# Performance work log

Measured on AMD Instinct MI355X. Metric: run time of the kernel, lower is better.

The kernel has to match this reference:

```python
import jax, jax.numpy as jnp
import numpy as np

B, L, D, H, HD = 2, 8192, 1024, 16, 64
MINI = 64
NC = L // MINI
TTT_BASE_LR = 1.0
NUM_CHUNKS = 4
TEXT_LEN = 64
INIT_OFFSET = 2048


def setup_inputs() -> dict:
    key = jax.random.key(0)
    ks = jax.random.split(key, 16)
    hidden_states = jax.random.normal(ks[0], (B, L, D), dtype=jnp.float32)
    # llama-style rope table as (cos, sin) pairs: [L, HD//2, 2]
    inv_freq = 1.0 / (10000.0 ** (np.arange(0, HD, 2, dtype=np.float32) / HD))
    t = np.arange(L, dtype=np.float32)
    ang = np.outer(t, inv_freq)  # [L, HD//2]
    freqs_cis = jnp.asarray(np.stack([np.cos(ang), np.sin(ang)], axis=-1))
    std = 0.02
    inp = {"hidden_states": hidden_states, "freqs_cis": freqs_cis}
    names = ["wq", "wk", "wv", "wu"]
    for i, n in enumerate(names):
        inp[n + "_w"] = jax.random.normal(ks[1 + i], (D, D), dtype=jnp.float32) * std  # [in, out]
        inp[n + "_b"] = jnp.zeros((D,), dtype=jnp.float32)
    inp["ttt_norm_weight"] = jnp.ones((H, HD), dtype=jnp.float32)
    inp["ttt_norm_bias"] = jnp.zeros((H, HD), dtype=jnp.float32)
    inp["lr_weight"] = jax.random.normal(ks[6], (H, 1, D), dtype=jnp.float32) * std
    inp["lr_bias"] = jnp.zeros((H, 1), dtype=jnp.float32)
    return inp


def _l2norm(x):
    return x / jnp.maximum(jnp.linalg.norm(x, axis=-1, keepdims=True), 1e-12)


def _rope(x, cos, sin):
    # x: [B, L, H, HD]; cos/sin: [L, HD//2] -> broadcast [1, L, 1, HD//2]
    c = cos[None, :, None, :]
    s = sin[None, :, None, :]
    xr, xi = x[..., 0::2], x[..., 1::2]
    out_r = xr * c - xi * s
    out_i = xr * s + xi * c
    return jnp.stack([out_r, out_i], axis=-1).reshape(x.shape)


def _interleave(x):
    # x: [B, H, NC, C, F]; splice text chunks into video scenes (static offsets)
    b, h, nc, c, f = x.shape
    xf = x.reshape(b, h, nc * c, f)
    stl = TEXT_LEN * NUM_CHUNKS
    x_text = xf[:, :, :stl]
    x_video = xf[:, :, stl:]
    texts = jnp.split(x_text, NUM_CHUNKS, axis=2)
    vio = INIT_OFFSET - TEXT_LEN
    vids = [x_video[:, :, :vio]] + list(jnp.split(x_video[:, :, vio:], NUM_CHUNKS - 1, axis=2))
    pieces = [jnp.concatenate([texts[i], vids[i]], axis=2) for i in range(NUM_CHUNKS)]
    return jnp.concatenate(pieces, axis=2).reshape(b, h, nc, c, f)


def reference(hidden_states, freqs_cis, wq_w, wq_b, wk_w, wk_b, wv_w, wv_b,
              wu_w, wu_b, ttt_norm_weight, ttt_norm_bias, lr_weight, lr_bias):
    X = hidden_states  # [B, L, D]
    XQ = (X @ wq_w + wq_b).reshape(B, L, H, HD)
    XK = (X @ wk_w + wk_b).reshape(B, L, H, HD)
    XV = (X @ wv_w + wv_b).reshape(B, L, H, HD)
    XU = (X @ wu_w + wu_b).reshape(B, L, H, HD)

    XQ, XK, XU = _l2norm(XQ), _l2norm(XK), _l2norm(XU)

    # seq_text_length = 0 in process_input -> rope over the whole sequence
    cos, sin = freqs_cis[..., 0], freqs_cis[..., 1]
    XQ = _rope(XQ, cos, sin)
    XK = _rope(XK, cos, sin)
    XU = _rope(XU, cos, sin)

    # ln reconstruction target (std uses Bessel correction like torch.std)
    diff = XV - XK
    mean = diff.mean(axis=-1, keepdims=True)
    std = jnp.std(diff, axis=-1, keepdims=True, ddof=1)
    norm = (diff - mean) / (std + 1e-8)
    XV = ttt_norm_weight[None, None] * norm + ttt_norm_bias[None, None] + XK

    # reshape to mini-batches: [B, H, NC, C, HD]
    def to_mb(t):
        return t.transpose(0, 2, 1, 3).reshape(B, H, NC, MINI, HD)
    XQ, XK, XV, XU = to_mb(XQ), to_mb(XK), to_mb(XV), to_mb(XU)
    Xmb = X.reshape(B, NC, MINI, D)

    # per-head LR gating
    ttt_lr = jnp.einsum('bnkc,hdc->bhnkd', Xmb, lr_weight) + lr_bias.reshape(1, -1, 1, 1, 1)
    ttt_lr = jax.nn.sigmoid(ttt_lr).transpose(0, 1, 2, 4, 3)  # [B, H, NC, 1, C]
    ttt_lr = TTT_BASE_LR * ttt_lr / HD
    eta = (1.0 / MINI) * jnp.tile(ttt_lr, (1, 1, 1, MINI, 1))  # [B, H, NC, C, C]

    XQ, XK, XV, XU = _interleave(XQ), _interleave(XK), _interleave(XV), _interleave(XU)
    eta = _interleave(eta)

    # HD == MINI == 64 so all five stack cleanly
    return jnp.stack([XQ, XK, XV, XU, eta], axis=0)
```

## Files before the change

### kernel.cpp

```cpp
#include <hip/hip_runtime.h>

typedef unsigned int u32;
typedef unsigned short u16;
typedef short short8v __attribute__((ext_vector_type(8)));
typedef float f32x4 __attribute__((ext_vector_type(4)));

#define ND 1024
#define NH 16
#define OUT_T ((size_t)16777216)

__device__ __forceinline__ u16 f2bf(float f) {
  u32 u = __float_as_uint(f);
  u32 r = u + 0x7fffu + ((u >> 16) & 1u);
  return (u16)(r >> 16);
}

__device__ __forceinline__ short8v pack8(float4 a, float4 b) {
  short8v v;
  v[0] = (short)f2bf(a.x); v[1] = (short)f2bf(a.y);
  v[2] = (short)f2bf(a.z); v[3] = (short)f2bf(a.w);
  v[4] = (short)f2bf(b.x); v[5] = (short)f2bf(b.y);
  v[6] = (short)f2bf(b.z); v[7] = (short)f2bf(b.w);
  return v;
}

__device__ __forceinline__ void st8(float* p, const float* v) {
  for (int i = 0; i < 2; ++i) {
    f32x4 t; t[0] = v[4*i]; t[1] = v[4*i+1]; t[2] = v[4*i+2]; t[3] = v[4*i+3];
    *(f32x4*)(p + 4*i) = t;
  }
}

__device__ __forceinline__ void gload16(const void* g, void* l) {
  __builtin_amdgcn_global_load_lds((const __attribute__((address_space(1))) void*)g,
                                   (__attribute__((address_space(3))) void*)l, 16, 0, 0);
}

__global__ void k_wt(const float* __restrict__ w0, const float* __restrict__ w1,
                     const float* __restrict__ w2, const float* __restrict__ w3,
                     u16* __restrict__ WT) {
  __shared__ float T[64][65];
  int bid = blockIdx.x;
  int w = bid >> 8;
  int tk = (bid >> 4) & 15, tc = bid & 15;
  const float* W = w == 0 ? w0 : w == 1 ? w1 : w == 2 ? w2 : w3;
  int k0 = tk << 6, c0 = tc << 6;
  int tid = threadIdx.x;
  for (int it = 0; it < 16; ++it) {
    int idx = it * 256 + tid;
    int kk = idx >> 6, cc = idx & 63;
    T[kk][cc] = W[(size_t)(k0 + kk) * ND + c0 + cc];
  }
  __syncthreads();
  for (int it = 0; it < 2; ++it) {
    int ci = it * 256 + tid;
    int cc = ci >> 3, k8 = ci & 7;
    int c = c0 + cc;
    short8v v;
    for (int j = 0; j < 8; ++j) v[j] = (short)f2bf(T[k8 * 8 + j][cc]);
    size_t off = ((size_t)(w * ND + c) << 10) + k0 + (((k8 ^ c) & 7) << 3);
    *(short8v*)(WT + off) = v;
  }
}

__global__ void k_xbf(const float* __restrict__ X, u16* __restrict__ Xb) {
  size_t i = ((size_t)blockIdx.x * 256 + threadIdx.x) * 8;
  float4 a = *(const float4*)(X + i), b = *(const float4*)(X + i + 4);
  *(short8v*)(Xb + i) = pack8(a, b);
}

__global__ __launch_bounds__(256) void k_lr2(const u16* __restrict__ Xb,
                                             const float* __restrict__ LW,
                                             const float* __restrict__ LB,
                                             float* __restrict__ out) {
  __shared__ __align__(16) char smem[46080];
  u16* LWs = (u16*)smem;
  u16* As = (u16*)(smem + 32768);
  float* El = (float*)(smem + 40960);
  const int tid = threadIdx.x, lane = tid & 63, wid = tid >> 6;
  const int l15 = lane & 15, lg = lane >> 4;
  const int n = blockIdx.x;
  const int tok0 = n << 6;

  {
    int row = tid >> 4;
    int cbase = (tid & 15) << 3;
    const float* src = LW + row * ND + (cbase << 3);
    for (int i = 0; i < 8; ++i) {
      float4 a = *(const float4*)(src + i * 8);
      float4 b = *(const float4*)(src + i * 8 + 4);
      int sc = (cbase + i) ^ (row & 7);
      *(short8v*)(LWs + row * 1024 + (sc << 3)) = pack8(a, b);
    }
  }

  const int arow0 = (wid << 4) + (lane >> 3);
  const u16* asrc = Xb + (size_t)(tok0 + arow0) * ND + ((((lane & 7) ^ arow0) & 7) << 3);
  const u32 aldo = wid << 10;
  const int aoff = ((wid << 4) + l15) << 6;
  const int key = l15 & 7;

  f32x4 acc;
  for (int r = 0; r < 4; ++r) acc[r] = 0.f;
  __syncthreads();

  for (int kt = 0; kt < 16; ++kt) {
    gload16(asrc + (kt << 6), As + aldo);
    gload16(asrc + (kt << 6) + 8 * ND, As + aldo + 512);
    __syncthreads();
    for (int ks = 0; ks < 2; ++ks) {
      int kcl = (ks << 2) + lg;
      int kcg = (kt << 3) + kcl;
      short8v af = *(const short8v*)(As + aoff + ((kcl ^ key) << 3));
      short8v bf = *(const short8v*)(LWs + (l15 << 10) + ((kcg ^ key) << 3));
      acc = __builtin_amdgcn_mfma_f32_16x16x32_bf16(af, bf, acc, 0, 0, 0);
    }
    __syncthreads();
  }

  for (int rr = 0; rr < 4; ++rr) {
    float v = acc[rr] + LB[l15];
    float e = (1.f / (1.f + expf(-v))) * (1.f / 4096.f);
    El[l15 * 72 + (wid << 4) + (lg << 2) + rr] = e;
  }
  __syncthreads();

  const int b = n >> 7, nl = n & 127;
  int q, rc;
  if (nl < 4) { q = nl; rc = 0; }
  else { q = (nl - 4) / 31; rc = nl - 3 - 31 * q; }
  const int pc = q * 32 + rc;
  const int j = tid >> 2, kq = tid & 3;
  size_t base = 4 * OUT_T + (((size_t)(b * NH) << 13) + (pc << 6)) * 64 + (size_t)j * 64;
  for (int h = 0; h < 16; ++h) {
    float* po = out + base + ((size_t)h << 19);
    for (int qq = 0; qq < 4; ++qq) {
      int k0 = (kq + (qq << 2)) << 2;
      const float* ep = El + h * 72 + k0;
      f32x4 t; t[0] = ep[0]; t[1] = ep[1]; t[2] = ep[2]; t[3] = ep[3];
      *(f32x4*)(po + k0) = t;
    }
  }
}

__global__ __launch_bounds__(512, 2) void k_main(
    const u16* __restrict__ Xb, const float* __restrict__ FC,
    const u16* __restrict__ WT,
    const float* __restrict__ qb, const float* __restrict__ kb,
    const float* __restrict__ vb, const float* __restrict__ ub,
    const float* __restrict__ tw, const float* __restrict__ tb,
    float* __restrict__ out) {
  __shared__ __align__(16) char smem[131072];
  float* Cs = (float*)smem;

  const int tid = threadIdx.x;
  const int lane = tid & 63;
  const int wid = tid >> 6;
  const int wm = wid >> 2, wn = wid & 3;
  const int l15 = lane & 15, lg = lane >> 4;
  const int xcd = blockIdx.x & 7;
  const int local = blockIdx.x >> 3;
  const int h = (xcd << 1) | (local >> 6);
  const int s0 = (local & 63) << 8;

  f32x4 acc[8][4];
  for (int i = 0; i < 8; ++i)
    for (int j = 0; j < 4; ++j)
      for (int r = 0; r < 4; ++r) acc[i][j][r] = 0.f;

  const float* bp = (wn == 0) ? qb : (wn == 1) ? kb : (wn == 2) ? vb : ub;
  float biasv[4];
  for (int fn = 0; fn < 4; ++fn) biasv[fn] = bp[h * 64 + fn * 16 + l15];

  const int arow0 = (wid << 5) + (lane >> 3);
  const u16* asrc = Xb + (size_t)(s0 + arow0) * ND + ((((lane & 7) ^ arow0) & 7) << 3);
  const u32 aldo = wid << 11;
  const int brow_d = ((wid & 1) << 5) + (lane >> 3);
  const u16* bsrc = WT + (((size_t)((wid >> 1) * ND + h * 64 + brow_d)) << 10) + ((lane & 7) << 3);
  const u32 bldo = wid << 11;

  int aoff[8], akey[8], boff[4], bkey[4];
  for (int f = 0; f < 8; ++f) {
    int ra = (wm << 7) + (f << 4) + l15;
    aoff[f] = ra << 6; akey[f] = ra & 7;
  }
  for (int f = 0; f < 4; ++f) {
    int rb = (wn << 6) + (f << 4) + l15;
    boff[f] = rb << 6; bkey[f] = rb & 7;
  }

  for (int j = 0; j < 4; ++j) {
    gload16(asrc + j * (8 * ND), (u16*)smem + aldo + (j << 9));
    gload16(bsrc + j * 8192, (u16*)(smem + 32768) + bldo + (j << 9));
  }
  __syncthreads();

  for (int kt = 0; kt < 16; ++kt) {
    const int cur = kt & 1;
    if (kt < 15) {
      const int k0 = (kt + 1) << 6;
      u16* ad = (u16*)(smem + ((cur ^ 1) << 16));
      u16* bd = (u16*)(smem + 32768 + ((cur ^ 1) << 16));
      for (int j = 0; j < 4; ++j) {
        gload16(asrc + k0 + j * (8 * ND), ad + aldo + (j << 9));
        gload16(bsrc + k0 + j * 8192, bd + bldo + (j << 9));
      }
    }
    const u16* As = (const u16*)(smem + (cur << 16));
    const u16* Bs = (const u16*)(smem + 32768 + (cur << 16));
    for (int ks = 0; ks < 2; ++ks) {
      const int kc = (ks << 2) + lg;
      short8v af[8], bf[4];
      for (int f = 0; f < 8; ++f)
        af[f] = *(const short8v*)(As + aoff[f] + ((kc ^ akey[f]) << 3));
      for (int f = 0; f < 4; ++f)
        bf[f] = *(const short8v*)(Bs + boff[f] + ((kc ^ bkey[f]) << 3));
      for (int fm = 0; fm < 8; ++fm)
        for (int fn = 0; fn < 4; ++fn)
          acc[fm][fn] = __builtin_amdgcn_mfma_f32_16x16x32_bf16(
              af[fm], bf[fn], acc[fm][fn], 0, 0, 0);
    }
    __syncthreads();
  }

  for (int ph = 0; ph < 4; ++ph) {
    if (wm == (ph >> 1)) {
      for (int f2 = 0; f2 < 4; ++f2) {
        int fm = ((ph & 1) << 2) + f2;
        for (int fn = 0; fn < 4; ++fn)
          for (int rr = 0; rr < 4; ++rr) {
            int rl = (f2 << 4) + (lg << 2) + rr;
            int col = (wn << 6) + (fn << 4) + l15;
            Cs[rl * 261 + col] = acc[fm][fn][rr] + biasv[fn];
          }
      }
    }
    __syncthreads();
    {
      int tloc = tid >> 3, o = tid & 7;
      int dbase = o << 3;
      int stok = s0 + (ph << 6) + tloc;
      int b = stok >> 13, seq = stok & 8191;
      const float* crow = Cs + tloc * 261;
      float fc[8];
      {
        const f32x4* fp = (const f32x4*)(FC + ((size_t)seq << 6) + dbase);
        f32x4 t0 = fp[0], t1 = fp[1];
        fc[0] = t0[0]; fc[1] = t0[1]; fc[2] = t0[2]; fc[3] = t0[3];
        fc[4] = t1[0]; fc[5] = t1[1]; fc[6] = t1[2]; fc[7] = t1[3];
      }
      float sq = 0.f, sk = 0.f, su = 0.f;
      for (int j = 0; j < 8; ++j) {
        float a = crow[dbase + j], b2 = crow[64 + dbase + j], c = crow[192 + dbase + j];
        sq += a * a; sk += b2 * b2; su += c * c;
      }
      sq += __shfl_xor(sq, 1); sq += __shfl_xor(sq, 2); sq += __shfl_xor(sq, 4);
      sk += __shfl_xor(sk, 1); sk += __shfl_xor(sk, 2); sk += __shfl_xor(sk, 4);
      su += __shfl_xor(su, 1); su += __shfl_xor(su, 2); su += __shfl_xor(su, 4);
      float qi = 1.f / fmaxf(sqrtf(sq), 1e-12f);
      float ki = 1.f / fmaxf(sqrtf(sk), 1e-12f);
      float ui = 1.f / fmaxf(sqrtf(su), 1e-12f);
      int p;
      if (seq < 256) p = ((seq >> 6) << 11) + (seq & 63);
      else { int v = seq - 256; int qc = v / 1984; p = (qc << 11) + 64 + (v - qc * 1984); }
      float* po = out + ((((size_t)(b * NH + h) << 13) + p) << 6) + dbase;
      float kr[8];
      for (int jj = 0; jj < 4; ++jj) {
        float xa = crow[64 + dbase + 2*jj] * ki, xb = crow[64 + dbase + 2*jj + 1] * ki;
        float c = fc[2*jj], s = fc[2*jj+1];
        kr[2*jj]     = xa * c - xb * s;
        kr[2*jj + 1] = xa * s + xb * c;
      }
      st8(po + OUT_T, kr);
      float sd = 0.f, sdd = 0.f, df[8];
      for (int j = 0; j < 8; ++j) {
        df[j] = crow[128 + dbase + j] - kr[j];
        sd += df[j]; sdd += df[j] * df[j];
      }
      sd += __shfl_xor(sd, 1); sd += __shfl_xor(sd, 2); sd += __shfl_xor(sd, 4);
      sdd += __shfl_xor(sdd, 1); sdd += __shfl_xor(sdd, 2); sdd += __shfl_xor(sdd, 4);
      float mean = sd * (1.f / 64.f);
      float var = (sdd - sd * sd * (1.f / 64.f)) * (1.f / 63.f);
      float istd = 1.f / (sqrtf(fmaxf(var, 0.f)) + 1e-8f);
      for (int j = 0; j < 8; ++j) {
        int d = dbase + j;
        df[j] = tw[h * 64 + d] * ((df[j] - mean) * istd) + tb[h * 64 + d] + kr[j];
      }
      st8(po + 2 * OUT_T, df);
      float qr[8];
      for (int jj = 0; jj < 4; ++jj) {
        float xa = crow[dbase + 2*jj] * qi, xb = crow[dbase + 2*jj + 1] * qi;
        float c = fc[2*jj], s = fc[2*jj+1];
        qr[2*jj]     = xa * c - xb * s;
        qr[2*jj + 1] = xa * s + xb * c;
      }
      st8(po, qr);
      for (int jj = 0; jj < 4; ++jj) {
        float xa = crow[192 + dbase + 2*jj] * ui, xb = crow[192 + dbase + 2*jj + 1] * ui;
        float c = fc[2*jj], s = fc[2*jj+1];
        qr[2*jj]     = xa * c - xb * s;
        qr[2*jj + 1] = xa * s + xb * c;
      }
      st8(po + 3 * OUT_T, qr);
    }
    __syncthreads();
  }
}

extern "C" void kernel_launch(void* const* d_in, const int* in_sizes, int n_in,
                              void* d_out, int out_size, void* d_ws, size_t ws_size,
                              hipStream_t stream) {
  const float* X  = (const float*)d_in[0];
  const float* FC = (const float*)d_in[1];
  const float* wq = (const float*)d_in[2];
  const float* qb = (const float*)d_in[3];
  const float* wk = (const float*)d_in[4];
  const float* kb = (const float*)d_in[5];
  const float* wv = (const float*)d_in[6];
  const float* vb = (const float*)d_in[7];
  const float* wu = (const float*)d_in[8];
  const float* ub = (const float*)d_in[9];
  const float* tw = (const float*)d_in[10];
  const float* tb = (const float*)d_in[11];
  const float* lw = (const float*)d_in[12];
  const float* lb = (const float*)d_in[13];
  float* out = (float*)d_out;
  u16* WT = (u16*)d_ws;
  u16* Xb = (u16*)((char*)d_ws + (8u << 20));

  hipLaunchKernelGGL(k_wt, dim3(1024), dim3(256), 0, stream, wq, wk, wv, wu, WT);
  hipLaunchKernelGGL(k_xbf, dim3(8192), dim3(256), 0, stream, X, Xb);
  hipLaunchKernelGGL(k_lr2, dim3(256), dim3(256), 0, stream, Xb, lw, lb, out);
  hipLaunchKernelGGL(k_main, dim3(1024), dim3(512), 0, stream,
                     Xb, FC, WT, qb, kb, vb, ub, tw, tb, out);
}
```

Before: 230.1 us.

## Split GEMM k-step into four interleaved phases with explicit barriers and priority

The main GEMM k-loop is restructured into four quadrant phases. Each phase issues its LDS fragment reads and one slice of the next tile's global-to-LDS loads, then runs a block of MFMAs at raised wave priority, with explicit s_barrier, waitcnt and sched_barrier controlling the order. The aim is to overlap global loads and LDS reads with matrix math, replacing the coarse prefetch-then-compute-then-syncthreads pattern. This adds more barriers per iteration and always issues a redundant wrap-around prefetch on the last iteration, and it relies on the hand-placed waits being correct for LDS hazards.

```diff
diff --git a/kernel.cpp b/kernel.cpp
--- a/kernel.cpp
+++ b/kernel.cpp
@@ -8,6 +8,11 @@
 #define ND 1024
 #define NH 16
 #define OUT_T ((size_t)16777216)
+
+#define SBAR() __builtin_amdgcn_s_barrier()
+#define LGKM0() asm volatile("s_waitcnt lgkmcnt(0)" ::: "memory")
+#define VM0() asm volatile("s_waitcnt vmcnt(0)" ::: "memory")
+#define SCHED0() __builtin_amdgcn_sched_barrier(0)
 
 __device__ __forceinline__ u16 f2bf(float f) {
   u32 u = __float_as_uint(f);
@@ -193,34 +198,116 @@
     gload16(asrc + j * (8 * ND), (u16*)smem + aldo + (j << 9));
     gload16(bsrc + j * 8192, (u16*)(smem + 32768) + bldo + (j << 9));
   }
-  __syncthreads();
+  VM0();
+  SBAR();
 
   for (int kt = 0; kt < 16; ++kt) {
     const int cur = kt & 1;
-    if (kt < 15) {
-      const int k0 = (kt + 1) << 6;
-      u16* ad = (u16*)(smem + ((cur ^ 1) << 16));
-      u16* bd = (u16*)(smem + 32768 + ((cur ^ 1) << 16));
-      for (int j = 0; j < 4; ++j) {
-        gload16(asrc + k0 + j * (8 * ND), ad + aldo + (j << 9));
-        gload16(bsrc + k0 + j * 8192, bd + bldo + (j << 9));
-      }
-    }
     const u16* As = (const u16*)(smem + (cur << 16));
     const u16* Bs = (const u16*)(smem + 32768 + (cur << 16));
-    for (int ks = 0; ks < 2; ++ks) {
-      const int kc = (ks << 2) + lg;
-      short8v af[8], bf[4];
-      for (int f = 0; f < 8; ++f)
-        af[f] = *(const short8v*)(As + aoff[f] + ((kc ^ akey[f]) << 3));
-      for (int f = 0; f < 4; ++f)
-        bf[f] = *(const short8v*)(Bs + boff[f] + ((kc ^ bkey[f]) << 3));
-      for (int fm = 0; fm < 8; ++fm)
-        for (int fn = 0; fn < 4; ++fn)
+    u16* ad = (u16*)(smem + ((cur ^ 1) << 16));
+    u16* bd = (u16*)(smem + 32768 + ((cur ^ 1) << 16));
+    const int k0n = ((kt + 1) & 15) << 6;
+
+    short8v afA[4][2], afB[4][2], bfr[4][2];
+
+#pragma unroll
+    for (int f = 0; f < 4; ++f)
+#pragma unroll
+      for (int ks = 0; ks < 2; ++ks) {
+        int kc = (ks << 2) + lg;
+        afA[f][ks] = *(const short8v*)(As + aoff[f] + ((kc ^ akey[f]) << 3));
+      }
+#pragma unroll
+    for (int f = 0; f < 2; ++f)
+#pragma unroll
+      for (int ks = 0; ks < 2; ++ks) {
+        int kc = (ks << 2) + lg;
+        bfr[f][ks] = *(const short8v*)(Bs + boff[f] + ((kc ^ bkey[f]) << 3));
+      }
+    gload16(asrc + k0n, ad + aldo);
+    gload16(bsrc + k0n, bd + bldo);
+    SBAR();
+    LGKM0();
+    SCHED0();
+    __builtin_amdgcn_s_setprio(1);
+#pragma unroll
+    for (int fm = 0; fm < 4; ++fm)
+#pragma unroll
+      for (int fn = 0; fn < 2; ++fn)
+#pragma unroll
+        for (int ks = 0; ks < 2; ++ks)
           acc[fm][fn] = __builtin_amdgcn_mfma_f32_16x16x32_bf16(
-              af[fm], bf[fn], acc[fm][fn], 0, 0, 0);
-    }
-    __syncthreads();
+              afA[fm][ks], bfr[fn][ks], acc[fm][fn], 0, 0, 0);
+    __builtin_amdgcn_s_setprio(0);
+    SCHED0();
+    SBAR();
+
+#pragma unroll
+    for (int f = 2; f < 4; ++f)
+#pragma unroll
+      for (int ks = 0; ks < 2; ++ks) {
+        int kc = (ks << 2) + lg;
+        bfr[f][ks] = *(const short8v*)(Bs + boff[f] + ((kc ^ bkey[f]) << 3));
+      }
+    gload16(asrc + k0n + 8 * ND, ad + aldo + 512);
+    gload16(bsrc + k0n + 8192, bd + bldo + 512);
+    SBAR();
+    LGKM0();
+    SCHED0();
+    __builtin_amdgcn_s_setprio(1);
+#pragma unroll
+    for (int fm = 0; fm < 4; ++fm)
+#pragma unroll
+      for (int fn = 2; fn < 4; ++fn)
+#pragma unroll
+        for (int ks = 0; ks < 2; ++ks)
+          acc[fm][fn] = __builtin_amdgcn_mfma_f32_16x16x32_bf16(
+              afA[fm][ks], bfr[fn][ks], acc[fm][fn], 0, 0, 0);
+    __builtin_amdgcn_s_setprio(0);
+    SCHED0();
+    SBAR();
+
+#pragma unroll
+    for (int f = 0; f < 4; ++f)
+#pragma unroll
+      for (int ks = 0; ks < 2; ++ks) {
+        int kc = (ks << 2) + lg;
+        afB[f][ks] = *(const short8v*)(As + aoff[f + 4] + ((kc ^ akey[f + 4]) << 3));
+      }
+    gload16(asrc + k0n + 16 * ND, ad + aldo + 1024);
+    gload16(bsrc + k0n + 16384, bd + bldo + 1024);
+    SBAR();
+    LGKM0();
+    SCHED0();
+    __builtin_amdgcn_s_setprio(1);
+#pragma unroll
+    for (int fm = 0; fm < 4; ++fm)
+#pragma unroll
+      for (int fn = 0; fn < 2; ++fn)
+#pragma unroll
+        for (int ks = 0; ks < 2; ++ks)
+          acc[fm + 4][fn] = __builtin_amdgcn_mfma_f32_16x16x32_bf16(
+              afB[fm][ks], bfr[fn][ks], acc[fm + 4][fn], 0, 0, 0);
+    __builtin_amdgcn_s_setprio(0);
+    SCHED0();
+    SBAR();
+
+    gload16(asrc + k0n + 24 * ND, ad + aldo + 1536);
+    gload16(bsrc + k0n + 24576, bd + bldo + 1536);
+    __builtin_amdgcn_s_setprio(1);
+#pragma unroll
+    for (int fm = 0; fm < 4; ++fm)
+#pragma unroll
+      for (int fn = 2; fn < 4; ++fn)
+#pragma unroll
+        for (int ks = 0; ks < 2; ++ks)
+          acc[fm + 4][fn] = __builtin_amdgcn_mfma_f32_16x16x32_bf16(
+              afB[fm][ks], bfr[fn][ks], acc[fm + 4][fn], 0, 0, 0);
+    __builtin_amdgcn_s_setprio(0);
+    SCHED0();
+    VM0();
+    SBAR();
   }
 
   for (int ph = 0; ph < 4; ++ph) {
```

After: 231.2 us. No clear change (+0.5%).

## Restructure GEMM main loop into 4-stage ring with split loads and setprio

Applied to the files above, without the earlier changes.

Replaces the double-buffered 64-wide K tile loop with a 32-wide K tile, four-slot shared-memory ring that prefetches two tiles ahead. Each iteration splits the MFMA work into two halves interleaved with the A and B global loads, using explicit vmcnt waits, raw barriers and s_setprio to keep matrix units busy while loads are in flight. The LDS swizzle is changed to a 4-chunk XOR pattern to match the narrower rows, and the weight transpose kernel is updated to store in the same layout. This adds more barriers per K step and relies on hand-tuned waitcnt counts being correct.

```diff
diff --git a/kernel.cpp b/kernel.cpp
--- a/kernel.cpp
+++ b/kernel.cpp
@@ -8,6 +8,9 @@
 #define ND 1024
 #define NH 16
 #define OUT_T ((size_t)16777216)
+
+#define SBAR() __builtin_amdgcn_s_barrier()
+#define VMW(n) asm volatile("s_waitcnt vmcnt(" #n ")" ::: "memory")
 
 __device__ __forceinline__ u16 f2bf(float f) {
   u32 u = __float_as_uint(f);
@@ -58,7 +61,8 @@
     int c = c0 + cc;
     short8v v;
     for (int j = 0; j < 8; ++j) v[j] = (short)f2bf(T[k8 * 8 + j][cc]);
-    size_t off = ((size_t)(w * ND + c) << 10) + k0 + (((k8 ^ c) & 7) << 3);
+    int stored = (k8 & 4) | ((k8 ^ (c >> 1)) & 3);
+    size_t off = ((size_t)(w * ND + c) << 10) + k0 + (stored << 3);
     *(short8v*)(WT + off) = v;
   }
 }
@@ -160,7 +164,7 @@
   const int l15 = lane & 15, lg = lane >> 4;
   const int xcd = blockIdx.x & 7;
   const int local = blockIdx.x >> 3;
-  const int h = (xcd << 1) | (local >> 6);
+  const int h = (xcd << 1) | ((local >> 6) & 1);
   const int s0 = (local & 63) << 8;
 
   f32x4 acc[8][4];
@@ -172,55 +176,84 @@
   float biasv[4];
   for (int fn = 0; fn < 4; ++fn) biasv[fn] = bp[h * 64 + fn * 16 + l15];
 
-  const int arow0 = (wid << 5) + (lane >> 3);
-  const u16* asrc = Xb + (size_t)(s0 + arow0) * ND + ((((lane & 7) ^ arow0) & 7) << 3);
-  const u32 aldo = wid << 11;
-  const int brow_d = ((wid & 1) << 5) + (lane >> 3);
-  const u16* bsrc = WT + (((size_t)((wid >> 1) * ND + h * 64 + brow_d)) << 10) + ((lane & 7) << 3);
-  const u32 bldo = wid << 11;
+  const int rS = (wid << 4) + (lane >> 2);
+  const int chp = lane & 3;
+  const u16* asrc = Xb + (size_t)(s0 + rS) * ND + ((chp ^ ((rS >> 1) & 3)) << 3);
+  const u16* bsrc = WT + (((size_t)((rS >> 6) * ND + h * 64 + (rS & 63))) << 10) + (chp << 3);
+  const u32 ldo = wid << 9;
 
   int aoff[8], akey[8], boff[4], bkey[4];
   for (int f = 0; f < 8; ++f) {
     int ra = (wm << 7) + (f << 4) + l15;
-    aoff[f] = ra << 6; akey[f] = ra & 7;
+    aoff[f] = ra << 5; akey[f] = (ra >> 1) & 3;
   }
   for (int f = 0; f < 4; ++f) {
     int rb = (wn << 6) + (f << 4) + l15;
-    boff[f] = rb << 6; bkey[f] = rb & 7;
-  }
-
-  for (int j = 0; j < 4; ++j) {
-    gload16(asrc + j * (8 * ND), (u16*)smem + aldo + (j << 9));
-    gload16(bsrc + j * 8192, (u16*)(smem + 32768) + bldo + (j << 9));
-  }
-  __syncthreads();
-
-  for (int kt = 0; kt < 16; ++kt) {
-    const int cur = kt & 1;
-    if (kt < 15) {
-      const int k0 = (kt + 1) << 6;
-      u16* ad = (u16*)(smem + ((cur ^ 1) << 16));
-      u16* bd = (u16*)(smem + 32768 + ((cur ^ 1) << 16));
-      for (int j = 0; j < 4; ++j) {
-        gload16(asrc + k0 + j * (8 * ND), ad + aldo + (j << 9));
-        gload16(bsrc + k0 + j * 8192, bd + bldo + (j << 9));
-      }
-    }
-    const u16* As = (const u16*)(smem + (cur << 16));
-    const u16* Bs = (const u16*)(smem + 32768 + (cur << 16));
-    for (int ks = 0; ks < 2; ++ks) {
-      const int kc = (ks << 2) + lg;
-      short8v af[8], bf[4];
-      for (int f = 0; f < 8; ++f)
-        af[f] = *(const short8v*)(As + aoff[f] + ((kc ^ akey[f]) << 3));
-      for (int f = 0; f < 4; ++f)
-        bf[f] = *(const short8v*)(Bs + boff[f] + ((kc ^ bkey[f]) << 3));
-      for (int fm = 0; fm < 8; ++fm)
-        for (int fn = 0; fn < 4; ++fn)
-          acc[fm][fn] = __builtin_amdgcn_mfma_f32_16x16x32_bf16(
-              af[fm], bf[fn], acc[fm][fn], 0, 0, 0);
-    }
-    __syncthreads();
+    boff[f] = rb << 5; bkey[f] = (rb >> 1) & 3;
+  }
+
+  for (int t = 0; t < 2; ++t) {
+    const int k0 = t << 5;
+    u16* ad = (u16*)smem + (t << 13);
+    u16* bd = (u16*)smem + 32768 + (t << 13);
+    gload16(asrc + k0, ad + ldo);
+    gload16(asrc + k0 + 128 * ND, ad + ldo + 4096);
+    gload16(bsrc + k0, bd + ldo);
+    gload16(bsrc + k0 + 2097152, bd + ldo + 4096);
+  }
+  VMW(4);
+  SBAR();
+
+  for (int kt = 0; kt < 32; ++kt) {
+    const u16* As = (const u16*)smem + ((kt & 3) << 13);
+    const u16* Bs = (const u16*)smem + 32768 + ((kt & 3) << 13);
+    const int tp = kt + 2;
+    const int k0p = tp << 5;
+    u16* ad = (u16*)smem + ((tp & 3) << 13);
+    u16* bd = (u16*)smem + 32768 + ((tp & 3) << 13);
+
+    short8v afl[4], bfr[4];
+#pragma unroll
+    for (int f = 0; f < 4; ++f)
+      afl[f] = *(const short8v*)(As + aoff[f] + ((lg ^ akey[f]) << 3));
+#pragma unroll
+    for (int f = 0; f < 4; ++f)
+      bfr[f] = *(const short8v*)(Bs + boff[f] + ((lg ^ bkey[f]) << 3));
+    if (tp < 32) {
+      gload16(asrc + k0p, ad + ldo);
+      gload16(asrc + k0p + 128 * ND, ad + ldo + 4096);
+    }
+    SBAR();
+    __builtin_amdgcn_s_setprio(1);
+#pragma unroll
+    for (int fm = 0; fm < 4; ++fm)
+#pragma unroll
+      for (int fn = 0; fn < 4; ++fn)
+        acc[fm][fn] = __builtin_amdgcn_mfma_f32_16x16x32_bf16(
+            afl[fm], bfr[fn], acc[fm][fn], 0, 0, 0);
+    __builtin_amdgcn_s_setprio(0);
+    SBAR();
+
+    short8v afh[4];
+#pragma unroll
+    for (int f = 0; f < 4; ++f)
+      afh[f] = *(const short8v*)(As + aoff[f + 4] + ((lg ^ akey[f + 4]) << 3));
+    if (tp < 32) {
+      gload16(bsrc + k0p, bd + ldo);
+      gload16(bsrc + k0p + 2097152, bd + ldo + 4096);
+    }
+    SBAR();
+    __builtin_amdgcn_s_setprio(1);
+#pragma unroll
+    for (int fm = 0; fm < 4; ++fm)
+#pragma unroll
+      for (int fn = 0; fn < 4; ++fn)
+        acc[fm + 4][fn] = __builtin_amdgcn_mfma_f32_16x16x32_bf16(
+            afh[fm], bfr[fn], acc[fm + 4][fn], 0, 0, 0);
+    __builtin_amdgcn_s_setprio(0);
+    if (kt < 30) { VMW(4); }
+    else if (kt == 30) { VMW(0); }
+    SBAR();
   }
 
   for (int ph = 0; ph < 4; ++ph) {
```

Result: slower. 240.2 us (+4.4%).

## Rewrite projection GEMM main loop as 8-wave ping-pong schedule with explicit barriers

Applied to the files above, without the earlier changes.

Replaces the simple double-buffered K loop in the fused QKVU projection kernel with a hand-scheduled pipeline. Global-to-LDS loads are split into half-tile stages interleaved between MFMA quarter-blocks, with explicit s_waitcnt, s_barrier, sched_barrier and setprio around the MFMAs. The weight-transpose layout and the block-to-(head, sequence) mapping change to match the new LDS tiling, and the st8 helper is inlined. The aim is to overlap memory latency with matrix math and cut the stalls of the per-iteration full sync. In exchange it adds many barriers and more complex indexing that must stay correct.

```diff
diff --git a/kernel.cpp b/kernel.cpp
--- a/kernel.cpp
+++ b/kernel.cpp
@@ -8,6 +8,13 @@
 #define ND 1024
 #define NH 16
 #define OUT_T ((size_t)16777216)
+
+#define SBAR() __builtin_amdgcn_s_barrier()
+#define VMW(n) asm volatile("s_waitcnt vmcnt(" #n ")" ::: "memory")
+#define LGKM0() asm volatile("s_waitcnt lgkmcnt(0)" ::: "memory")
+#define SCHED0() __builtin_amdgcn_sched_barrier(0)
+#define PRIO1 __builtin_amdgcn_s_setprio(1)
+#define PRIO0 __builtin_amdgcn_s_setprio(0)
 
 __device__ __forceinline__ u16 f2bf(float f) {
   u32 u = __float_as_uint(f);
@@ -22,13 +29,6 @@
   v[4] = (short)f2bf(b.x); v[5] = (short)f2bf(b.y);
   v[6] = (short)f2bf(b.z); v[7] = (short)f2bf(b.w);
   return v;
-}
-
-__device__ __forceinline__ void st8(float* p, const float* v) {
-  for (int i = 0; i < 2; ++i) {
-    f32x4 t; t[0] = v[4*i]; t[1] = v[4*i+1]; t[2] = v[4*i+2]; t[3] = v[4*i+3];
-    *(f32x4*)(p + 4*i) = t;
-  }
 }
 
 __device__ __forceinline__ void gload16(const void* g, void* l) {
@@ -55,10 +55,10 @@
   for (int it = 0; it < 2; ++it) {
     int ci = it * 256 + tid;
     int cc = ci >> 3, k8 = ci & 7;
-    int c = c0 + cc;
     short8v v;
     for (int j = 0; j < 8; ++j) v[j] = (short)f2bf(T[k8 * 8 + j][cc]);
-    size_t off = ((size_t)(w * ND + c) << 10) + k0 + (((k8 ^ c) & 7) << 3);
+    size_t off = ((size_t)((w * 16 + tc) * 64 + cc)) * 1024 +
+                 ((tk << 3) + (k8 ^ (cc & 7))) * 8;
     *(short8v*)(WT + off) = v;
   }
 }
@@ -160,8 +160,8 @@
   const int l15 = lane & 15, lg = lane >> 4;
   const int xcd = blockIdx.x & 7;
   const int local = blockIdx.x >> 3;
-  const int h = (xcd << 1) | (local >> 6);
-  const int s0 = (local & 63) << 8;
+  const int h = (xcd << 1) | (local & 1);
+  const int s0 = (local >> 1) << 8;
 
   f32x4 acc[8][4];
   for (int i = 0; i < 8; ++i)
@@ -172,56 +172,113 @@
   float biasv[4];
   for (int fn = 0; fn < 4; ++fn) biasv[fn] = bp[h * 64 + fn * 16 + l15];
 
-  const int arow0 = (wid << 5) + (lane >> 3);
-  const u16* asrc = Xb + (size_t)(s0 + arow0) * ND + ((((lane & 7) ^ arow0) & 7) << 3);
-  const u32 aldo = wid << 11;
-  const int brow_d = ((wid & 1) << 5) + (lane >> 3);
-  const u16* bsrc = WT + (((size_t)((wid >> 1) * ND + h * 64 + brow_d)) << 10) + ((lane & 7) << 3);
-  const u32 bldo = wid << 11;
-
-  int aoff[8], akey[8], boff[4], bkey[4];
-  for (int f = 0; f < 8; ++f) {
-    int ra = (wm << 7) + (f << 4) + l15;
-    aoff[f] = ra << 6; akey[f] = ra & 7;
-  }
-  for (int f = 0; f < 4; ++f) {
-    int rb = (wn << 6) + (f << 4) + l15;
-    boff[f] = rb << 6; bkey[f] = rb & 7;
-  }
-
-  for (int j = 0; j < 4; ++j) {
-    gload16(asrc + j * (8 * ND), (u16*)smem + aldo + (j << 9));
-    gload16(bsrc + j * 8192, (u16*)(smem + 32768) + bldo + (j << 9));
-  }
-  __syncthreads();
-
-  for (int kt = 0; kt < 16; ++kt) {
-    const int cur = kt & 1;
-    if (kt < 15) {
-      const int k0 = (kt + 1) << 6;
-      u16* ad = (u16*)(smem + ((cur ^ 1) << 16));
-      u16* bd = (u16*)(smem + 32768 + ((cur ^ 1) << 16));
-      for (int j = 0; j < 4; ++j) {
-        gload16(asrc + k0 + j * (8 * ND), ad + aldo + (j << 9));
-        gload16(bsrc + k0 + j * 8192, bd + bldo + (j << 9));
-      }
-    }
-    const u16* As = (const u16*)(smem + (cur << 16));
-    const u16* Bs = (const u16*)(smem + 32768 + (cur << 16));
-    for (int ks = 0; ks < 2; ++ks) {
-      const int kc = (ks << 2) + lg;
-      short8v af[8], bf[4];
-      for (int f = 0; f < 8; ++f)
-        af[f] = *(const short8v*)(As + aoff[f] + ((kc ^ akey[f]) << 3));
-      for (int f = 0; f < 4; ++f)
-        bf[f] = *(const short8v*)(Bs + boff[f] + ((kc ^ bkey[f]) << 3));
-      for (int fm = 0; fm < 8; ++fm)
-        for (int fn = 0; fn < 4; ++fn)
-          acc[fm][fn] = __builtin_amdgcn_mfma_f32_16x16x32_bf16(
-              af[fm], bf[fn], acc[fm][fn], 0, 0, 0);
-    }
-    __syncthreads();
-  }
+  const u16* asrc_t = Xb + (size_t)(s0 + (tid >> 3)) * ND +
+                      (((tid & 7) ^ ((tid >> 3) & 7)) << 3);
+  const u16* bsrc_t = WT + ((size_t)h * 64 + (tid >> 3)) * 1024 + ((tid & 7) << 3);
+  const u32 awo = wid << 9;
+
+  int aoff[8], boff[4], akx[2];
+  for (int f = 0; f < 8; ++f) aoff[f] = ((wm << 7) + (f << 4) + l15) << 6;
+  for (int f = 0; f < 4; ++f) boff[f] = 16384 + (((wn << 6) + (f << 4) + l15) << 6);
+  for (int ks = 0; ks < 2; ++ks) akx[ks] = (((ks << 2) + lg) ^ (l15 & 7)) << 3;
+
+#define STAGE_A(b, t, hf) do { \
+    gload16(asrc_t + (size_t)(((hf) << 7)) * ND + ((t) << 6), \
+            (u16*)smem + ((b) << 15) + ((hf) << 13) + awo); \
+    gload16(asrc_t + (size_t)(((hf) << 7) + 64) * ND + ((t) << 6), \
+            (u16*)smem + ((b) << 15) + ((hf) << 13) + 4096 + awo); \
+  } while (0)
+
+#define STAGE_B(b, t, hf) do { \
+    gload16(bsrc_t + (size_t)((hf) * 2) * 1048576 + ((t) << 6), \
+            (u16*)smem + ((b) << 15) + 16384 + ((hf) << 13) + awo); \
+    gload16(bsrc_t + (size_t)((hf) * 2 + 1) * 1048576 + ((t) << 6), \
+            (u16*)smem + ((b) << 15) + 16384 + ((hf) << 13) + 4096 + awo); \
+  } while (0)
+
+#define RD_A4(dst, b, flo) do { \
+    const u16* _p = (const u16*)smem + ((b) << 15); \
+    _Pragma("unroll") \
+    for (int f = 0; f < 4; ++f) \
+      _Pragma("unroll") \
+      for (int ks = 0; ks < 2; ++ks) \
+        dst[f][ks] = *(const short8v*)(_p + aoff[(flo) + f] + akx[ks]); \
+  } while (0)
+
+#define RD_B2(dst, b, flo) do { \
+    const u16* _p = (const u16*)smem + ((b) << 15); \
+    _Pragma("unroll") \
+    for (int f = 0; f < 2; ++f) \
+      _Pragma("unroll") \
+      for (int ks = 0; ks < 2; ++ks) \
+        dst[f][ks] = *(const short8v*)(_p + boff[(flo) + f] + akx[ks]); \
+  } while (0)
+
+#define MM(af, bf, fmb, fnb) do { \
+    PRIO1; \
+    _Pragma("unroll") \
+    for (int fm = 0; fm < 4; ++fm) \
+      _Pragma("unroll") \
+      for (int fn = 0; fn < 2; ++fn) \
+        _Pragma("unroll") \
+        for (int ks = 0; ks < 2; ++ks) \
+          acc[(fmb) + fm][(fnb) + fn] = __builtin_amdgcn_mfma_f32_16x16x32_bf16( \
+              af[fm][ks], bf[fn][ks], acc[(fmb) + fm][(fnb) + fn], 0, 0, 0); \
+    PRIO0; \
+  } while (0)
+
+  STAGE_B(0, 0, 0); STAGE_B(0, 0, 1);
+  STAGE_A(0, 0, 0); STAGE_A(0, 0, 1);
+  STAGE_B(1, 1, 0); STAGE_B(1, 1, 1);
+  VMW(4);
+  SBAR();
+
+  short8v afA[4][2], afB[4][2], bfL[2][2], bfH[2][2];
+  for (int i = 0; i < 8; ++i) {
+    const int e = i << 1;
+    RD_A4(afA, 0, 0);
+    RD_B2(bfL, 0, 0);
+    STAGE_A(1, e + 1, 0);
+    SBAR(); LGKM0(); SCHED0();
+    MM(afA, bfL, 0, 0);
+    SBAR();
+    RD_B2(bfH, 0, 2);
+    STAGE_A(1, e + 1, 1);
+    SBAR(); LGKM0(); SCHED0();
+    MM(afA, bfH, 0, 2);
+    SBAR();
+    RD_A4(afB, 0, 4);
+    if (i < 7) STAGE_B(0, e + 2, 0);
+    SBAR(); LGKM0(); SCHED0();
+    MM(afB, bfL, 4, 0);
+    SBAR();
+    if (i < 7) STAGE_B(0, e + 2, 1);
+    MM(afB, bfH, 4, 2);
+    if (i < 7) { VMW(4); } else { VMW(0); }
+    SBAR();
+    RD_A4(afA, 1, 0);
+    RD_B2(bfL, 1, 0);
+    if (i < 7) STAGE_A(0, e + 2, 0);
+    SBAR(); LGKM0(); SCHED0();
+    MM(afA, bfL, 0, 0);
+    SBAR();
+    RD_B2(bfH, 1, 2);
+    if (i < 7) STAGE_A(0, e + 2, 1);
+    SBAR(); LGKM0(); SCHED0();
+    MM(afA, bfH, 0, 2);
+    SBAR();
+    RD_A4(afB, 1, 4);
+    if (i < 7) STAGE_B(1, e + 3, 0);
+    SBAR(); LGKM0(); SCHED0();
+    MM(afB, bfL, 4, 0);
+    SBAR();
+    if (i < 7) STAGE_B(1, e + 3, 1);
+    MM(afB, bfH, 4, 2);
+    if (i < 7) { VMW(4); }
+    SBAR();
+  }
+  VMW(0); LGKM0();
+  SBAR();
 
   for (int ph = 0; ph < 4; ++ph) {
     if (wm == (ph >> 1)) {
@@ -271,7 +328,10 @@
         kr[2*jj]     = xa * c - xb * s;
         kr[2*jj + 1] = xa * s + xb * c;
       }
-      st8(po + OUT_T, kr);
+      for (int i2 = 0; i2 < 2; ++i2) {
+        f32x4 t; t[0] = kr[4*i2]; t[1] = kr[4*i2+1]; t[2] = kr[4*i2+2]; t[3] = kr[4*i2+3];
+        *(f32x4*)(po + OUT_T + 4*i2) = t;
+      }
       float sd = 0.f, sdd = 0.f, df[8];
       for (int j = 0; j < 8; ++j) {
         df[j] = crow[128 + dbase + j] - kr[j];
@@ -286,7 +346,10 @@
         int d = dbase + j;
         df[j] = tw[h * 64 + d] * ((df[j] - mean) * istd) + tb[h * 64 + d] + kr[j];
       }
-      st8(po + 2 * OUT_T, df);
+      for (int i2 = 0; i2 < 2; ++i2) {
+        f32x4 t; t[0] = df[4*i2]; t[1] = df[4*i2+1]; t[2] = df[4*i2+2]; t[3] = df[4*i2+3];
+        *(f32x4*)(po + 2 * OUT_T + 4*i2) = t;
+      }
       float qr[8];
       for (int jj = 0; jj < 4; ++jj) {
         float xa = crow[dbase + 2*jj] * qi, xb = crow[dbase + 2*jj + 1] * qi;
@@ -294,14 +357,20 @@
         qr[2*jj]     = xa * c - xb * s;
         qr[2*jj + 1] = xa * s + xb * c;
       }
-      st8(po, qr);
+      for (int i2 = 0; i2 < 2; ++i2) {
+        f32x4 t; t[0] = qr[4*i2]; t[1] = qr[4*i2+1]; t[2] = qr[4*i2+2]; t[3] = qr[4*i2+3];
+        *(f32x4*)(po + 4*i2) = t;
+      }
       for (int jj = 0; jj < 4; ++jj) {
         float xa = crow[192 + dbase + 2*jj] * ui, xb = crow[192 + dbase + 2*jj + 1] * ui;
         float c = fc[2*jj], s = fc[2*jj+1];
         qr[2*jj]     = xa * c - xb * s;
         qr[2*jj + 1] = xa * s + xb * c;
       }
-      st8(po + 3 * OUT_T, qr);
+      for (int i2 = 0; i2 < 2; ++i2) {
+        f32x4 t; t[0] = qr[4*i2]; t[1] = qr[4*i2+1]; t[2] = qr[4*i2+2]; t[3] = qr[4*i2+3];
+        *(f32x4*)(po + 3 * OUT_T + 4*i2) = t;
+      }
     }
     __syncthreads();
   }
```

After: 227.6 us. No clear change (-1.1%).
